# Optimization experiments

Measured on AMD Instinct MI355X. Metric: run time of the kernel, lower is better.

Reference implementation:

```python
import jax, jax.numpy as jnp
import numpy as np

_EPS = 1e-8

# Stacked Sobel kernels, pre-divided by 8 (matches conv2d(...)/8.0 in torch).
# Shape: (O=2, I=1, 3, 3); channel 0 = sobel_x, channel 1 = sobel_y.
_SOBEL = jnp.stack([
    jnp.array([[-1.0, 0.0, 1.0], [-2.0, 0.0, 2.0], [-1.0, 0.0, 1.0]], jnp.float32),
    jnp.array([[-1.0, -2.0, -1.0], [0.0, 0.0, 0.0], [1.0, 2.0, 1.0]], jnp.float32),
])[:, None, :, :] / 8.0


def setup_inputs() -> dict:
    key = jax.random.key(0)
    k1, k2 = jax.random.split(key)
    B, C, H, W = 64, 1, 512, 512
    pred_dist = jax.random.uniform(k1, (B, C, H, W), dtype=jnp.float32) * 10.0
    reachable = jax.random.uniform(k2, (B, C, H, W), dtype=jnp.float32)
    return {"pred_dist": pred_dist, "reachable": reachable}


def reference(pred_dist, reachable) -> jnp.ndarray:
    # Replicate (edge) padding, as F.pad(..., mode='replicate')
    padded = jnp.pad(pred_dist, ((0, 0), (0, 0), (1, 1), (1, 1)), mode="edge")
    # Single conv with 2 output channels computes grad_x and grad_y together.
    grads = jax.lax.conv_general_dilated(
        padded, _SOBEL.astype(pred_dist.dtype),
        window_strides=(1, 1), padding="VALID",
        dimension_numbers=("NCHW", "OIHW", "NCHW"),
    )  # [B, 2, H, W]
    gx = grads[:, 0:1]
    gy = grads[:, 1:2]
    magnitude = jnp.sqrt(gx * gx + gy * gy + _EPS)
    violation = jnp.abs(magnitude - 1.0)
    mask = (reachable > 0.5).astype(violation.dtype)
    denom = jnp.maximum(mask.sum(), 1.0)
    return (violation * mask).sum() / denom
```

## Files before the change

kernel.cpp:

```cpp
#include <hip/hip_runtime.h>
#include <math.h>

#define HW   512
#define IMG  (512 * 512)
#define NB   64
#define BLOCK 256
#define WAVES_PER_BLOCK (BLOCK / 64)
#define TOTAL_ROWS (NB * HW)
#define NBLOCKS    (TOTAL_ROWS / WAVES_PER_BLOCK)

__global__ __launch_bounds__(BLOCK) void eik_main(const float* __restrict__ pred,
                                                  const float* __restrict__ reach,
                                                  float* __restrict__ partials) {
    const int lane = threadIdx.x & 63;
    const int w    = blockIdx.x * WAVES_PER_BLOCK + (threadIdx.x >> 6);
    const int y    = w & (HW - 1);
    const int b    = w >> 9;

    const int ym = (y > 0)      ? y - 1 : 0;
    const int yp = (y < HW - 1) ? y + 1 : HW - 1;

    const float* base = pred + (size_t)b * IMG;
    const float* pm = base + (size_t)ym * HW + (lane << 3);
    const float* p0 = base + (size_t)y  * HW + (lane << 3);
    const float* pp = base + (size_t)yp * HW + (lane << 3);
    const float* rp = reach + (size_t)b * IMG + (size_t)y * HW + (lane << 3);

    const float4 m0 = *(const float4*)pm;
    const float4 m1 = *(const float4*)(pm + 4);
    const float4 c0 = *(const float4*)p0;
    const float4 c1 = *(const float4*)(p0 + 4);
    const float4 q0 = *(const float4*)pp;
    const float4 q1 = *(const float4*)(pp + 4);
    const float4 r0 = *(const float4*)rp;
    const float4 r1 = *(const float4*)(rp + 4);

    const float am[8] = {m0.x, m0.y, m0.z, m0.w, m1.x, m1.y, m1.z, m1.w};
    const float a0[8] = {c0.x, c0.y, c0.z, c0.w, c1.x, c1.y, c1.z, c1.w};
    const float ap[8] = {q0.x, q0.y, q0.z, q0.w, q1.x, q1.y, q1.z, q1.w};
    const float rv[8] = {r0.x, r0.y, r0.z, r0.w, r1.x, r1.y, r1.z, r1.w};

    float s[8], d[8];
#pragma unroll
    for (int i = 0; i < 8; ++i) {
        s[i] = am[i] + 2.0f * a0[i] + ap[i];
        d[i] = ap[i] - am[i];
    }

    float sl = __shfl_up(s[7], 1, 64);
    float dl = __shfl_up(d[7], 1, 64);
    float sr = __shfl_down(s[0], 1, 64);
    float dr = __shfl_down(d[0], 1, 64);
    if (lane == 0)  { sl = s[0]; dl = d[0]; }
    if (lane == 63) { sr = s[7]; dr = d[7]; }

    const float S[10] = {sl, s[0], s[1], s[2], s[3], s[4], s[5], s[6], s[7], sr};
    const float D[10] = {dl, d[0], d[1], d[2], d[3], d[4], d[5], d[6], d[7], dr};

    float vsum = 0.0f, csum = 0.0f;
#pragma unroll
    for (int i = 0; i < 8; ++i) {
        const float gx = (S[i+2] - S[i]) * 0.125f;
        const float gy = (D[i] + 2.0f * D[i+1] + D[i+2]) * 0.125f;
        const float mag  = sqrtf(gx * gx + gy * gy + 1e-8f);
        const float viol = fabsf(mag - 1.0f);
        const bool  m    = rv[i] > 0.5f;
        vsum += m ? viol : 0.0f;
        csum += m ? 1.0f : 0.0f;
    }

#pragma unroll
    for (int off = 32; off > 0; off >>= 1) {
        vsum += __shfl_down(vsum, off, 64);
        csum += __shfl_down(csum, off, 64);
    }

    __shared__ float sv[WAVES_PER_BLOCK];
    __shared__ float sc[WAVES_PER_BLOCK];
    const int wid = threadIdx.x >> 6;
    if (lane == 0) { sv[wid] = vsum; sc[wid] = csum; }
    __syncthreads();
    if (threadIdx.x == 0) {
        partials[2 * blockIdx.x]     = sv[0] + sv[1] + sv[2] + sv[3];
        partials[2 * blockIdx.x + 1] = sc[0] + sc[1] + sc[2] + sc[3];
    }
}

__global__ __launch_bounds__(BLOCK) void eik_finalize(const float* __restrict__ partials,
                                                      float* __restrict__ out) {
    float v = 0.0f, c = 0.0f;
    for (int i = threadIdx.x; i < NBLOCKS; i += BLOCK) {
        v += partials[2 * i];
        c += partials[2 * i + 1];
    }
#pragma unroll
    for (int off = 32; off > 0; off >>= 1) {
        v += __shfl_down(v, off, 64);
        c += __shfl_down(c, off, 64);
    }
    __shared__ float sv[WAVES_PER_BLOCK];
    __shared__ float sc[WAVES_PER_BLOCK];
    const int lane = threadIdx.x & 63;
    const int wid  = threadIdx.x >> 6;
    if (lane == 0) { sv[wid] = v; sc[wid] = c; }
    __syncthreads();
    if (threadIdx.x == 0) {
        const float vt = sv[0] + sv[1] + sv[2] + sv[3];
        const float ct = sc[0] + sc[1] + sc[2] + sc[3];
        out[0] = vt / fmaxf(ct, 1.0f);
    }
}

extern "C" void kernel_launch(void* const* d_in, const int* in_sizes, int n_in,
                              void* d_out, int out_size, void* d_ws, size_t ws_size,
                              hipStream_t stream) {
    const float* pred  = (const float*)d_in[0];
    const float* reach = (const float*)d_in[1];
    float* out = (float*)d_out;
    float* ws  = (float*)d_ws;

    eik_main<<<NBLOCKS, BLOCK, 0, stream>>>(pred, reach, ws);
    eik_finalize<<<1, BLOCK, 0, stream>>>(ws, out);
}
```

Baseline: 150.0 us.

## Process four rows per wave with register row reuse and fast sqrt

Each wave now handles four consecutive output rows and loads the six input rows it needs once into registers, where before every output row loaded three rows. This cuts redundant loads of pred from roughly 3x to 1.5x and shrinks the grid and the partials array by four. It also swaps sqrtf for the AMDGCN sqrt builtin to avoid the precise-sqrt sequence, trading a little accuracy. Register pressure goes up and there are fewer waves to hide memory latency.

```diff
diff --git a/kernel.cpp b/kernel.cpp
--- a/kernel.cpp
+++ b/kernel.cpp
@@ -4,69 +4,83 @@
 #define HW   512
 #define IMG  (512 * 512)
 #define NB   64
+#define T    4
 #define BLOCK 256
 #define WAVES_PER_BLOCK (BLOCK / 64)
-#define TOTAL_ROWS (NB * HW)
-#define NBLOCKS    (TOTAL_ROWS / WAVES_PER_BLOCK)
+#define WAVES_PER_IMG (HW / T)
+#define TOTAL_WAVES (NB * WAVES_PER_IMG)
+#define NBLOCKS     (TOTAL_WAVES / WAVES_PER_BLOCK)
+
+__device__ __forceinline__ void unpack8(const float4& q0, const float4& q1, float* a) {
+    a[0] = q0.x; a[1] = q0.y; a[2] = q0.z; a[3] = q0.w;
+    a[4] = q1.x; a[5] = q1.y; a[6] = q1.z; a[7] = q1.w;
+}
 
 __global__ __launch_bounds__(BLOCK) void eik_main(const float* __restrict__ pred,
                                                   const float* __restrict__ reach,
                                                   float* __restrict__ partials) {
     const int lane = threadIdx.x & 63;
     const int w    = blockIdx.x * WAVES_PER_BLOCK + (threadIdx.x >> 6);
-    const int y    = w & (HW - 1);
-    const int b    = w >> 9;
-
-    const int ym = (y > 0)      ? y - 1 : 0;
-    const int yp = (y < HW - 1) ? y + 1 : HW - 1;
+    const int y0   = (w & (WAVES_PER_IMG - 1)) * T;
+    const int b    = w >> 7;
+    const int xo   = lane << 3;
 
     const float* base = pred + (size_t)b * IMG;
-    const float* pm = base + (size_t)ym * HW + (lane << 3);
-    const float* p0 = base + (size_t)y  * HW + (lane << 3);
-    const float* pp = base + (size_t)yp * HW + (lane << 3);
-    const float* rp = reach + (size_t)b * IMG + (size_t)y * HW + (lane << 3);
 
-    const float4 m0 = *(const float4*)pm;
-    const float4 m1 = *(const float4*)(pm + 4);
-    const float4 c0 = *(const float4*)p0;
-    const float4 c1 = *(const float4*)(p0 + 4);
-    const float4 q0 = *(const float4*)pp;
-    const float4 q1 = *(const float4*)(pp + 4);
-    const float4 r0 = *(const float4*)rp;
-    const float4 r1 = *(const float4*)(rp + 4);
-
-    const float am[8] = {m0.x, m0.y, m0.z, m0.w, m1.x, m1.y, m1.z, m1.w};
-    const float a0[8] = {c0.x, c0.y, c0.z, c0.w, c1.x, c1.y, c1.z, c1.w};
-    const float ap[8] = {q0.x, q0.y, q0.z, q0.w, q1.x, q1.y, q1.z, q1.w};
-    const float rv[8] = {r0.x, r0.y, r0.z, r0.w, r1.x, r1.y, r1.z, r1.w};
-
-    float s[8], d[8];
+    float4 P[6][2];
 #pragma unroll
-    for (int i = 0; i < 8; ++i) {
-        s[i] = am[i] + 2.0f * a0[i] + ap[i];
-        d[i] = ap[i] - am[i];
+    for (int j = 0; j < 6; ++j) {
+        int r = y0 - 1 + j;
+        r = r < 0 ? 0 : (r > HW - 1 ? HW - 1 : r);
+        const float* p = base + (size_t)r * HW + xo;
+        P[j][0] = *(const float4*)p;
+        P[j][1] = *(const float4*)(p + 4);
+    }
+    float4 R[T][2];
+    const float* rbase = reach + (size_t)b * IMG + (size_t)y0 * HW + xo;
+#pragma unroll
+    for (int t = 0; t < T; ++t) {
+        R[t][0] = *(const float4*)(rbase + (size_t)t * HW);
+        R[t][1] = *(const float4*)(rbase + (size_t)t * HW + 4);
     }
 
-    float sl = __shfl_up(s[7], 1, 64);
-    float dl = __shfl_up(d[7], 1, 64);
-    float sr = __shfl_down(s[0], 1, 64);
-    float dr = __shfl_down(d[0], 1, 64);
-    if (lane == 0)  { sl = s[0]; dl = d[0]; }
-    if (lane == 63) { sr = s[7]; dr = d[7]; }
+    float vsum = 0.0f, csum = 0.0f;
 
-    const float S[10] = {sl, s[0], s[1], s[2], s[3], s[4], s[5], s[6], s[7], sr};
-    const float D[10] = {dl, d[0], d[1], d[2], d[3], d[4], d[5], d[6], d[7], dr};
+#pragma unroll
+    for (int t = 0; t < T; ++t) {
+        float am[8], a0[8], ap[8], rv[8];
+        unpack8(P[t][0],     P[t][1],     am);
+        unpack8(P[t + 1][0], P[t + 1][1], a0);
+        unpack8(P[t + 2][0], P[t + 2][1], ap);
+        unpack8(R[t][0],     R[t][1],     rv);
 
-    float vsum = 0.0f, csum = 0.0f;
+        float s[8], d[8];
 #pragma unroll
-    for (int i = 0; i < 8; ++i) {
-        const float gx = (S[i+2] - S[i]) * 0.125f;
-        const float gy = (D[i] + 2.0f * D[i+1] + D[i+2]) * 0.125f;
-        const float mag  = sqrtf(gx * gx + gy * gy + 1e-8f);
-        const float viol = fabsf(mag - 1.0f);
-        const bool  m    = rv[i] > 0.5f;
-        vsum += m ? viol : 0.0f;
-        csum += m ? 1.0f : 0.0f;
+        for (int i = 0; i < 8; ++i) {
+            s[i] = am[i] + 2.0f * a0[i] + ap[i];
+            d[i] = ap[i] - am[i];
+        }
+
+        float sl = __shfl_up(s[7], 1, 64);
+        float dl = __shfl_up(d[7], 1, 64);
+        float sr = __shfl_down(s[0], 1, 64);
+        float dr = __shfl_down(d[0], 1, 64);
+        if (lane == 0)  { sl = s[0]; dl = d[0]; }
+        if (lane == 63) { sr = s[7]; dr = d[7]; }
+
+        const float S[10] = {sl, s[0], s[1], s[2], s[3], s[4], s[5], s[6], s[7], sr};
+        const float D[10] = {dl, d[0], d[1], d[2], d[3], d[4], d[5], d[6], d[7], dr};
+
+#pragma unroll
+        for (int i = 0; i < 8; ++i) {
+            const float gx = (S[i+2] - S[i]) * 0.125f;
+            const float gy = (D[i] + 2.0f * D[i+1] + D[i+2]) * 0.125f;
+            const float mag  = __builtin_amdgcn_sqrtf(gx * gx + gy * gy + 1e-8f);
+            const float viol = fabsf(mag - 1.0f);
+            const bool  m    = rv[i] > 0.5f;
+            vsum += m ? viol : 0.0f;
+            csum += m ? 1.0f : 0.0f;
+        }
     }
 
 #pragma unroll
```

Result: faster. 146.7 us (-2.2%).
